# Kernel tuning notes

Measured on AMD Instinct MI355X. Metric: run time of the kernel, lower is better.

The kernel has to match this reference:

```python
import jax, jax.numpy as jnp
import numpy as np

# Ordered bi-bi mechanism, species order per _build_species_list:
# [E, EA, EQ, EAB, A, B, P, Q] -> indices 0..7
# Transitions: E+A<->EA, EA+B<->EAB, EAB<->EQ+P, EQ<->E+Q (all reversible)
N_SPECIES = 8
N_TRANS = 4

# forward: rate * [enzyme] * prod([substrates]); -1 = no factor (padded)
ENZ_F = np.array([0, 1, 3, 2], dtype=np.int32)          # E, EA, EAB, EQ
SUB_F = np.array([[4], [5], [-1], [-1]], dtype=np.int32)  # A, B, -, -
# reverse: rate * [to-enzyme] * prod([products])
ENZ_R = np.array([1, 3, 2, 0], dtype=np.int32)          # EA, EAB, EQ, E
PROD_R = np.array([[-1], [-1], [6], [7]], dtype=np.int32)  # -, -, P, Q
REV_MASK = np.array([1.0, 1.0, 1.0, 1.0], dtype=np.float32)

# Stoichiometry (n_trans, n_species), applied as dydt += v_net[:,None]*S[i]
S_FORWARD = np.array([
    [-1,  1,  0,  0, -1,  0,  0,  0],
    [ 0, -1,  0,  1,  0, -1,  0,  0],
    [ 0,  0,  1, -1,  0,  0,  1,  0],
    [ 1,  0, -1,  0,  0,  0,  0,  1],
], dtype=np.float32)


def _masked_gather_prod(y, idx):
    # y: (B, n_species); idx: (n_trans, k) with -1 padding
    safe = jnp.maximum(idx, 0)
    g = y[:, safe.reshape(-1)].reshape(y.shape[0], idx.shape[0], idx.shape[1])  # (B,T,k)
    g = jnp.where(idx[None, :, :] >= 0, g, 1.0)
    return jnp.prod(g, axis=-1)  # (B, T)


def setup_inputs() -> dict:
    key = jax.random.key(0)
    k1, k2, k3 = jax.random.split(key, 3)
    B = 2_000_000
    return {
        "t": jnp.zeros((1,), dtype=jnp.float32),
        "y": jax.random.uniform(k1, (B, N_SPECIES), dtype=jnp.float32),
        "forward_rates": jax.random.uniform(k2, (B, N_TRANS), dtype=jnp.float32),
        "reverse_rates": jax.random.uniform(k3, (B, N_TRANS), dtype=jnp.float32),
    }


def reference(t, y, forward_rates, reverse_rates):
    enz_f = jnp.asarray(ENZ_F)
    enz_r = jnp.asarray(ENZ_R)
    sub_f = jnp.asarray(SUB_F)
    prod_r = jnp.asarray(PROD_R)
    S = jnp.asarray(S_FORWARD)
    rev_mask = jnp.asarray(REV_MASK)

    # v_forward[b,i] = k_f[b,i] * y[b, enz_f[i]] * prod_j y[b, sub_f[i,j]]
    v_f = forward_rates * y[:, enz_f] * _masked_gather_prod(y, sub_f)
    # v_reverse analogous, zeroed for irreversible transitions
    v_r = reverse_rates * y[:, enz_r] * _masked_gather_prod(y, prod_r) * rev_mask[None, :]
    v_net = v_f - v_r  # (B, T)
    # dydt[b,s] = sum_i v_net[b,i] * S[i,s]
    return jnp.einsum("bt,ts->bs", v_net, S)
```

## Files before the change

### kernel.cpp

```cpp
#include <hip/hip_runtime.h>


typedef float v4f __attribute__((ext_vector_type(4)));

__device__ __forceinline__ void ode_elem(v4f ya, v4f yb, v4f f, v4f r,
                                         v4f& oa, v4f& ob) {
    float E  = ya.x, EA = ya.y, EQ = ya.z, EAB = ya.w;
    float A  = yb.x, Bc = yb.y, P  = yb.z, Q   = yb.w;

    float v0 = f.x * E   * A  - r.x * EA;
    float v1 = f.y * EA  * Bc - r.y * EAB;
    float v2 = f.z * EAB      - r.z * EQ * P;
    float v3 = f.w * EQ       - r.w * E  * Q;

    oa.x = v3 - v0;
    oa.y = v0 - v1;
    oa.z = v2 - v3;
    oa.w = v1 - v2;
    ob.x = -v0;
    ob.y = -v1;
    ob.z =  v2;
    ob.w =  v3;
}

__global__ __launch_bounds__(256, 8) void ode_kernel(
    const v4f* __restrict__ y4,
    const v4f* __restrict__ kf4,
    const v4f* __restrict__ kr4,
    v4f* __restrict__ out4,
    int B)
{
    const int T = gridDim.x * blockDim.x;
    int e = blockIdx.x * blockDim.x + threadIdx.x;

    bool v = e < B;
    v4f ya, yb, f, r;
    if (v) {
        ya = y4[2 * e];
        yb = y4[2 * e + 1];
        f  = kf4[e];
        r  = kr4[e];
    }

    while (v) {
        int  en = e + T;
        bool vn = en < B;
        v4f yan, ybn, fn, rn;
        if (vn) {
            yan = y4[2 * en];
            ybn = y4[2 * en + 1];
            fn  = kf4[en];
            rn  = kr4[en];
        }

        v4f oa, ob;
        ode_elem(ya, yb, f, r, oa, ob);
        out4[2 * e]     = oa;
        out4[2 * e + 1] = ob;

        e = en; v = vn;
        ya = yan; yb = ybn; f = fn; r = rn;
    }
}

extern "C" void kernel_launch(void* const* d_in, const int* in_sizes, int n_in,
                              void* d_out, int out_size, void* d_ws, size_t ws_size,
                              hipStream_t stream) {
    const v4f* y4  = (const v4f*)d_in[1];
    const v4f* kf4 = (const v4f*)d_in[2];
    const v4f* kr4 = (const v4f*)d_in[3];
    v4f* out4 = (v4f*)d_out;
    int B = in_sizes[1] / 8;

    int block = 256;
    int grid  = 2048;
    int maxg  = (B + block - 1) / block;
    if (grid > maxg) grid = maxg;
    ode_kernel<<<grid, block, 0, stream>>>(y4, kf4, kr4, out4, B);
}
```

Baseline: 171.9 us.

## Stage y and output through LDS for unit-stride coalesced accesses, one element per thread

Replaces the grid-stride prefetching loop with a one-element-per-thread launch covering the whole batch. The y input and output are exchanged through shared memory so each global vector load and store is unit-stride across the block, instead of each thread touching two adjacent 16-byte vectors. This targets memory coalescing efficiency and raises the number of in-flight blocks. In exchange it adds two block barriers and LDS traffic, and drops the register double-buffering.

```diff
diff --git a/kernel.cpp b/kernel.cpp
--- a/kernel.cpp
+++ b/kernel.cpp
@@ -2,6 +2,8 @@
 
 
 typedef float v4f __attribute__((ext_vector_type(4)));
+
+#define TPB 256
 
 __device__ __forceinline__ void ode_elem(v4f ya, v4f yb, v4f f, v4f r,
                                          v4f& oa, v4f& ob) {
@@ -23,44 +25,45 @@
     ob.w =  v3;
 }
 
-__global__ __launch_bounds__(256, 8) void ode_kernel(
+__global__ __launch_bounds__(TPB) void ode_kernel(
     const v4f* __restrict__ y4,
     const v4f* __restrict__ kf4,
     const v4f* __restrict__ kr4,
     v4f* __restrict__ out4,
     int B)
 {
-    const int T = gridDim.x * blockDim.x;
-    int e = blockIdx.x * blockDim.x + threadIdx.x;
+    __shared__ v4f buf[2 * TPB];
 
-    bool v = e < B;
-    v4f ya, yb, f, r;
-    if (v) {
-        ya = y4[2 * e];
-        yb = y4[2 * e + 1];
-        f  = kf4[e];
-        r  = kr4[e];
-    }
+    const int tid  = threadIdx.x;
+    const int base = blockIdx.x * TPB;
+    const int n2   = 2 * B;
 
-    while (v) {
-        int  en = e + T;
-        bool vn = en < B;
-        v4f yan, ybn, fn, rn;
-        if (vn) {
-            yan = y4[2 * en];
-            ybn = y4[2 * en + 1];
-            fn  = kf4[en];
-            rn  = kr4[en];
-        }
+    const int gy0 = 2 * base + tid;
+    const int gy1 = gy0 + TPB;
+    const int e   = base + tid;
 
-        v4f oa, ob;
-        ode_elem(ya, yb, f, r, oa, ob);
-        out4[2 * e]     = oa;
-        out4[2 * e + 1] = ob;
+    v4f a0 = {0.f, 0.f, 0.f, 0.f}, a1 = {0.f, 0.f, 0.f, 0.f};
+    v4f f  = {0.f, 0.f, 0.f, 0.f}, r  = {0.f, 0.f, 0.f, 0.f};
+    if (gy0 < n2) a0 = y4[gy0];
+    if (gy1 < n2) a1 = y4[gy1];
+    if (e < B) { f = kf4[e]; r = kr4[e]; }
 
-        e = en; v = vn;
-        ya = yan; yb = ybn; f = fn; r = rn;
-    }
+    buf[tid]       = a0;
+    buf[tid + TPB] = a1;
+    __syncthreads();
+
+    v4f ya = buf[2 * tid];
+    v4f yb = buf[2 * tid + 1];
+
+    v4f oa, ob;
+    ode_elem(ya, yb, f, r, oa, ob);
+
+    buf[2 * tid]     = oa;
+    buf[2 * tid + 1] = ob;
+    __syncthreads();
+
+    if (gy0 < n2) out4[gy0] = buf[tid];
+    if (gy1 < n2) out4[gy1] = buf[tid + TPB];
 }
 
 extern "C" void kernel_launch(void* const* d_in, const int* in_sizes, int n_in,
@@ -72,9 +75,6 @@
     v4f* out4 = (v4f*)d_out;
     int B = in_sizes[1] / 8;
 
-    int block = 256;
-    int grid  = 2048;
-    int maxg  = (B + block - 1) / block;
-    if (grid > maxg) grid = maxg;
-    ode_kernel<<<grid, block, 0, stream>>>(y4, kf4, kr4, out4, B);
+    int grid = (B + TPB - 1) / TPB;
+    ode_kernel<<<grid, TPB, 0, stream>>>(y4, kf4, kr4, out4, B);
 }
```

After: 171.6 us. No clear change (-0.2%).
